# Kernel optimization log

Hardware: AMD Instinct MI355X
Metric: run time of the kernel (lower is better)

The kernel has to match this reference:

```python
import jax, jax.numpy as jnp
import numpy as np

B, S, D = 1, 4096, 512
QK_DIM, N_HEADS = 512, 8
HEAD_DIM = QK_DIM // N_HEADS


def setup_inputs() -> dict:
    key = jax.random.key(0)
    ks = jax.random.split(key, 9)
    s_in = 1.0 / np.sqrt(D)
    s_v = 1.0 / np.sqrt(QK_DIM)
    return {
        "x": jax.random.normal(ks[0], (B, S, D), dtype=jnp.float32),
        # torch nn.Linear convention: weight (out_features, in_features)
        "Wq": jax.random.uniform(ks[1], (QK_DIM, D), jnp.float32, -s_in, s_in),
        "bq": jax.random.uniform(ks[2], (QK_DIM,), jnp.float32, -s_in, s_in),
        "Wk": jax.random.uniform(ks[3], (QK_DIM, D), jnp.float32, -s_in, s_in),
        "bk": jax.random.uniform(ks[4], (QK_DIM,), jnp.float32, -s_in, s_in),
        "Wv": jax.random.uniform(ks[5], (QK_DIM, D), jnp.float32, -s_in, s_in),
        "bv": jax.random.uniform(ks[6], (QK_DIM,), jnp.float32, -s_in, s_in),
        "Wo": jax.random.uniform(ks[7], (D, QK_DIM), jnp.float32, -s_v, s_v),
        "bo": jax.random.uniform(ks[8], (D,), jnp.float32, -s_v, s_v),
    }


def reference(x, Wq, bq, Wk, bk, Wv, bv, Wo, bo):
    # Faithful to source: tokens flattened over batch*seq before head split.
    n = x.shape[0] * x.shape[1]  # B*S
    Q = (x @ Wq.T + bq).reshape(n, N_HEADS, HEAD_DIM).transpose(1, 0, 2)  # (H, N, hd)
    K = (x @ Wk.T + bk).reshape(n, N_HEADS, HEAD_DIM).transpose(1, 0, 2)
    V = (x @ Wv.T + bv).reshape(n, N_HEADS, HEAD_DIM).transpose(1, 0, 2)
    scores = jnp.einsum("hnd,hmd->hnm", Q, K) / np.sqrt(HEAD_DIM).astype(np.float32)
    attn = jax.nn.softmax(scores, axis=-1)                # (H, N, N) materialized
    ctx = jnp.einsum("hnm,hmd->hnd", attn, V)             # (H, N, hd)
    ctx = ctx.transpose(1, 0, 2).reshape(n, QK_DIM)       # (N, qk_dim)
    return ctx @ Wo.T + bo                                # (N, input_dim)
```

## Files before the change

### kernel.cpp

```cpp
#include <hip/hip_runtime.h>
#include <math.h>

#define N_TOK 4096
#define DMODEL 512
#define NH 8
#define HD 64

typedef __attribute__((ext_vector_type(4))) float f32x4;
typedef __attribute__((ext_vector_type(8))) _Float16 f16x8;
typedef __attribute__((ext_vector_type(4))) _Float16 f16x4;

#define MFMA16(A, B, C) __builtin_amdgcn_mfma_f32_16x16x32_f16(A, B, C, 0, 0, 0)

__global__ __launch_bounds__(256) void cast_x(const float* __restrict__ x,
                                              _Float16* __restrict__ X16) {
    int i = (blockIdx.x * 256 + threadIdx.x) * 8;
    f32x4 a = *(const f32x4*)&x[i];
    f32x4 b = *(const f32x4*)&x[i + 4];
    f16x8 o = {(_Float16)a[0], (_Float16)a[1], (_Float16)a[2], (_Float16)a[3],
               (_Float16)b[0], (_Float16)b[1], (_Float16)b[2], (_Float16)b[3]};
    *(f16x8*)&X16[i] = o;
}

__global__ __launch_bounds__(768) void qkv_gemm(const _Float16* __restrict__ X16,
                                                const float* __restrict__ Wq,
                                                const float* __restrict__ bq,
                                                const float* __restrict__ Wk,
                                                const float* __restrict__ bk,
                                                const float* __restrict__ Wv,
                                                const float* __restrict__ bv,
                                                _Float16* __restrict__ Q16,
                                                _Float16* __restrict__ K16,
                                                _Float16* __restrict__ VT16) {
    __shared__ __align__(16) _Float16 smem[46080];
    _Float16* AsB = smem;
    _Float16* WsB = smem + 18432;

    int t = threadIdx.x;
    int w = t >> 6, l = t & 63, quad = l >> 4, ln = l & 15;
    int z = w >> 2, ww = w & 3;
    int n0 = blockIdx.x * 128, o0 = blockIdx.y * 64;
    int h = o0 >> 6;

    const float* biasz = (z == 0) ? bq : (z == 1) ? bk : bv;

    f32x4 acc[2][4] = {};

    bool isA = (t < 256);
    int asr = t >> 3, asc = (t & 7) * 8;
    int tt = t - 256;
    int wr = tt >> 3, wc = (tt & 7) * 8;

    const _Float16* Abase = X16 + (size_t)n0 * DMODEL;
    const float* W0 = Wq + (size_t)o0 * DMODEL;
    const float* W1 = Wk + (size_t)o0 * DMODEL;
    const float* W2 = Wv + (size_t)o0 * DMODEL;

    f16x8 pa[4];
    f32x4 pw[3][2];
    if (isA) {
#pragma unroll
        for (int r = 0; r < 4; r++)
            pa[r] = *(const f16x8*)&Abase[(size_t)(asr + r * 32) * DMODEL + asc];
    } else {
        pw[0][0] = *(const f32x4*)&W0[(size_t)wr * DMODEL + wc];
        pw[0][1] = *(const f32x4*)&W0[(size_t)wr * DMODEL + wc + 4];
        pw[1][0] = *(const f32x4*)&W1[(size_t)wr * DMODEL + wc];
        pw[1][1] = *(const f32x4*)&W1[(size_t)wr * DMODEL + wc + 4];
        pw[2][0] = *(const f32x4*)&W2[(size_t)wr * DMODEL + wc];
        pw[2][1] = *(const f32x4*)&W2[(size_t)wr * DMODEL + wc + 4];
    }

    for (int it = 0; it < 8; it++) {
        int p = it & 1;
        if (isA) {
#pragma unroll
            for (int r = 0; r < 4; r++)
                *(f16x8*)&AsB[(size_t)(p * 128 + asr + r * 32) * 72 + asc] = pa[r];
        } else {
#pragma unroll
            for (int zt = 0; zt < 3; zt++) {
                f16x8 wv_ = {(_Float16)pw[zt][0][0], (_Float16)pw[zt][0][1],
                             (_Float16)pw[zt][0][2], (_Float16)pw[zt][0][3],
                             (_Float16)pw[zt][1][0], (_Float16)pw[zt][1][1],
                             (_Float16)pw[zt][1][2], (_Float16)pw[zt][1][3]};
                *(f16x8*)&WsB[(size_t)((p * 3 + zt) * 64 + wr) * 72 + wc] = wv_;
            }
        }
        __syncthreads();

        int k1 = (it + 1) * 64;
        if (k1 < DMODEL) {
            if (isA) {
#pragma unroll
                for (int r = 0; r < 4; r++)
                    pa[r] = *(const f16x8*)&Abase[(size_t)(asr + r * 32) * DMODEL + k1 + asc];
            } else {
                pw[0][0] = *(const f32x4*)&W0[(size_t)wr * DMODEL + k1 + wc];
                pw[0][1] = *(const f32x4*)&W0[(size_t)wr * DMODEL + k1 + wc + 4];
                pw[1][0] = *(const f32x4*)&W1[(size_t)wr * DMODEL + k1 + wc];
                pw[1][1] = *(const f32x4*)&W1[(size_t)wr * DMODEL + k1 + wc + 4];
                pw[2][0] = *(const f32x4*)&W2[(size_t)wr * DMODEL + k1 + wc];
                pw[2][1] = *(const f32x4*)&W2[(size_t)wr * DMODEL + k1 + wc + 4];
            }
        }

#pragma unroll
        for (int ks = 0; ks < 2; ks++) {
            f16x8 af0 = *(const f16x8*)&AsB[(size_t)(p * 128 + ww * 32 + ln) * 72 +
                                            ks * 32 + quad * 8];
            f16x8 af1 = *(const f16x8*)&AsB[(size_t)(p * 128 + ww * 32 + 16 + ln) * 72 +
                                            ks * 32 + quad * 8];
#pragma unroll
            for (int c = 0; c < 4; c++) {
                f16x8 bf = *(const f16x8*)&WsB[(size_t)((p * 3 + z) * 64 + c * 16 + ln) * 72 +
                                               ks * 32 + quad * 8];
                acc[0][c] = MFMA16(af0, bf, acc[0][c]);
                acc[1][c] = MFMA16(af1, bf, acc[1][c]);
            }
        }
    }

    __syncthreads();

    const float QS = 0.125f * 1.44269504088896340736f;
    _Float16* Qs = smem;
    _Float16* Ksep = smem + 9216;
    _Float16* Vt = smem + 18432;

    if (z < 2) {
        _Float16* st = (z == 0) ? Qs : Ksep;
        float sc_ = (z == 0) ? QS : 1.0f;
#pragma unroll
        for (int c = 0; c < 4; c++) {
            float bv_ = biasz[o0 + c * 16 + ln];
#pragma unroll
            for (int rt = 0; rt < 2; rt++)
#pragma unroll
                for (int i = 0; i < 4; i++) {
                    int lr = ww * 32 + rt * 16 + quad * 4 + i;
                    st[(size_t)lr * 72 + c * 16 + ln] =
                        (_Float16)((acc[rt][c][i] + bv_) * sc_);
                }
        }
    } else {
#pragma unroll
        for (int c = 0; c < 4; c++) {
            float bv_ = biasz[o0 + c * 16 + ln];
#pragma unroll
            for (int rt = 0; rt < 2; rt++)
#pragma unroll
                for (int i = 0; i < 4; i++) {
                    int np = (ww >> 1) * 64 + (quad * 4 + i) * 4 + (ww & 1) * 2 + rt;
                    Vt[(size_t)(c * 16 + ln) * 136 + np] = (_Float16)(acc[rt][c][i] + bv_);
                }
        }
    }
    __syncthreads();

    if (t < 256) {
#pragma unroll
        for (int k = 0; k < 4; k++) {
            int row = k * 32 + (t >> 3), col = (t & 7) * 8;
            *(f16x8*)&Q16[((size_t)h * N_TOK + n0 + row) * HD + col] =
                *(const f16x8*)&Qs[(size_t)row * 72 + col];
        }
    } else if (t < 512) {
        int u = t - 256;
#pragma unroll
        for (int k = 0; k < 4; k++) {
            int row = k * 32 + (u >> 3), col = (u & 7) * 8;
            *(f16x8*)&K16[((size_t)h * N_TOK + n0 + row) * HD + col] =
                *(const f16x8*)&Ksep[(size_t)row * 72 + col];
        }
    } else {
        int u = t - 512;
#pragma unroll
        for (int k = 0; k < 4; k++) {
            int d = k * 16 + (u >> 4), col = (u & 15) * 8;
            *(f16x8*)&VT16[((size_t)h * HD + d) * N_TOK + n0 + col] =
                *(const f16x8*)&Vt[(size_t)d * 136 + col];
        }
    }
}

#define SWZ(r, c) (((r) * 64) + ((c) ^ (((r) & 7) << 3)))

__global__ __launch_bounds__(1024) void flash_mfma(const _Float16* __restrict__ Q16,
                                                   const _Float16* __restrict__ K16,
                                                   const _Float16* __restrict__ VT16,
                                                   _Float16* __restrict__ OP,
                                                   float* __restrict__ LS) {
    __shared__ __align__(16) _Float16 Ks[2][64 * 64];
    __shared__ __align__(16) _Float16 Vs[2][64 * 64];
    __shared__ __align__(16) _Float16 Ps[16][32 * 64];

    int t = threadIdx.x;
    int w = t >> 6, l = t & 63, quad = l >> 4, ln = l & 15;
    int bid = blockIdx.x;
    int h = bid & 7;
    int qt = (bid >> 3) & 7;
    int s = bid >> 6;
    int q0 = qt * 512 + w * 32;
    int m_start = s * 1024;

    f16x8 qf[2][2];
#pragma unroll
    for (int rt = 0; rt < 2; rt++) {
        const _Float16* qp = &Q16[((size_t)h * N_TOK + q0 + rt * 16 + ln) * HD + quad * 8];
        qf[rt][0] = *(const f16x8*)qp;
        qf[rt][1] = *(const f16x8*)(qp + 32);
    }

    f32x4 oacc[2][4] = {};
    f32x4 lsum[2] = {};

    const _Float16* kbase = K16 + (size_t)h * N_TOK * HD;
    const _Float16* vbase = VT16 + (size_t)h * HD * N_TOK;
    int g = t >> 9, tt = t & 511;
    int srow = tt >> 3, scol = (tt & 7) * 8;

    f16x8 pkv;
    if (g == 0)
        pkv = *(const f16x8*)(kbase + (size_t)(m_start + srow) * HD + scol);
    else
        pkv = *(const f16x8*)(vbase + (size_t)srow * N_TOK + m_start + scol);

    for (int it = 0; it < 16; it++) {
        int m0 = m_start + it * 64;
        int p = it & 1;
        if (g == 0)
            *(f16x8*)&Ks[p][SWZ(srow, scol)] = pkv;
        else
            *(f16x8*)&Vs[p][SWZ(srow, scol)] = pkv;
        __syncthreads();

        if (it < 15) {
            int m1 = m0 + 64;
            if (g == 0)
                pkv = *(const f16x8*)(kbase + (size_t)(m1 + srow) * HD + scol);
            else
                pkv = *(const f16x8*)(vbase + (size_t)srow * N_TOK + m1 + scol);
        }

        f16x8 kb[4][2];
#pragma unroll
        for (int c = 0; c < 4; c++) {
            kb[c][0] = *(const f16x8*)&Ks[p][SWZ(c * 16 + ln, quad * 8)];
            kb[c][1] = *(const f16x8*)&Ks[p][SWZ(c * 16 + ln, 32 + quad * 8)];
        }
#pragma unroll
        for (int rt = 0; rt < 2; rt++) {
            f32x4 sacc[4] = {};
#pragma unroll
            for (int c = 0; c < 4; c++) {
                sacc[c] = MFMA16(qf[rt][0], kb[c][0], sacc[c]);
                sacc[c] = MFMA16(qf[rt][1], kb[c][1], sacc[c]);
            }
#pragma unroll
            for (int i = 0; i < 4; i++) {
                float p0 = __builtin_exp2f(sacc[0][i]);
                float p1 = __builtin_exp2f(sacc[1][i]);
                float p2 = __builtin_exp2f(sacc[2][i]);
                float p3 = __builtin_exp2f(sacc[3][i]);
                lsum[rt][i] += (p0 + p1) + (p2 + p3);
                f16x4 pvv = {(_Float16)p0, (_Float16)p1, (_Float16)p2, (_Float16)p3};
                *(f16x4*)&Ps[w][SWZ(rt * 16 + quad * 4 + i, ln * 4)] = pvv;
            }
        }
        f16x8 vb[4][2];
#pragma unroll
        for (int c = 0; c < 4; c++) {
            vb[c][0] = *(const f16x8*)&Vs[p][SWZ(c * 16 + ln, quad * 8)];
            vb[c][1] = *(const f16x8*)&Vs[p][SWZ(c * 16 + ln, 32 + quad * 8)];
        }
#pragma unroll
        for (int rt = 0; rt < 2; rt++) {
            f16x8 a0 = *(const f16x8*)&Ps[w][SWZ(rt * 16 + ln, quad * 8)];
            f16x8 a1 = *(const f16x8*)&Ps[w][SWZ(rt * 16 + ln, 32 + quad * 8)];
#pragma unroll
            for (int c = 0; c < 4; c++) {
                oacc[rt][c] = MFMA16(a0, vb[c][0], oacc[rt][c]);
                oacc[rt][c] = MFMA16(a1, vb[c][1], oacc[rt][c]);
            }
        }
    }

#pragma unroll
    for (int d = 1; d < 16; d <<= 1)
#pragma unroll
        for (int rt = 0; rt < 2; rt++)
#pragma unroll
            for (int i = 0; i < 4; i++) lsum[rt][i] += __shfl_xor(lsum[rt][i], d, 64);

    _Float16* obase = OP + (size_t)s * N_TOK * DMODEL;
#pragma unroll
    for (int rt = 0; rt < 2; rt++)
#pragma unroll
        for (int c = 0; c < 4; c++)
#pragma unroll
            for (int i = 0; i < 4; i++) {
                int r = q0 + rt * 16 + quad * 4 + i;
                obase[(size_t)r * DMODEL + h * HD + c * 16 + ln] = (_Float16)oacc[rt][c][i];
            }
    if (ln == 0) {
#pragma unroll
        for (int rt = 0; rt < 2; rt++)
#pragma unroll
            for (int i = 0; i < 4; i++) {
                int r = q0 + rt * 16 + quad * 4 + i;
                LS[((size_t)s * NH + h) * N_TOK + r] = lsum[rt][i];
            }
    }
}

__global__ __launch_bounds__(512) void out_gemm(const _Float16* __restrict__ OP,
                                                const float* __restrict__ LS,
                                                const float* __restrict__ Wo,
                                                const float* __restrict__ bo,
                                                float* __restrict__ out) {
    __shared__ __align__(16) _Float16 smem[27648];
    _Float16* AsB = smem;
    _Float16* WsB = smem + 18432;

    int t = threadIdx.x;
    int w = t >> 6, l = t & 63, quad = l >> 4, ln = l & 15;
    int n0 = blockIdx.x * 128, o0 = blockIdx.y * 64;
    int sr = t >> 2, sc = (t & 3) * 16;
    int wr = t >> 3, wc = (t & 7) * 8;
    const size_t PSTR = (size_t)N_TOK * DMODEL;

    f32x4 acc[4] = {};

    const float* Wbase = Wo + (size_t)o0 * DMODEL;

    f16x8 pa[4][2];
    float lt;
    f32x4 pw0, pw1;
    {
        size_t base = (size_t)(n0 + sr) * DMODEL + sc;
#pragma unroll
        for (int s_ = 0; s_ < 4; s_++) {
            pa[s_][0] = *(const f16x8*)&OP[s_ * PSTR + base];
            pa[s_][1] = *(const f16x8*)&OP[s_ * PSTR + base + 8];
        }
        const float* ls = LS + n0 + sr;
        lt = (ls[0] + ls[NH * N_TOK]) + (ls[2 * NH * N_TOK] + ls[3 * NH * N_TOK]);
        pw0 = *(const f32x4*)&Wbase[(size_t)wr * DMODEL + wc];
        pw1 = *(const f32x4*)&Wbase[(size_t)wr * DMODEL + wc + 4];
    }

    for (int it = 0; it < 8; it++) {
        int p = it & 1;
        {
            float inv = 1.0f / lt;
            f16x8 s0, s1;
#pragma unroll
            for (int j = 0; j < 8; j++) {
                s0[j] = (_Float16)(
                    ((((float)pa[0][0][j] + (float)pa[1][0][j]) +
                      ((float)pa[2][0][j] + (float)pa[3][0][j]))) * inv);
                s1[j] = (_Float16)(
                    ((((float)pa[0][1][j] + (float)pa[1][1][j]) +
                      ((float)pa[2][1][j] + (float)pa[3][1][j]))) * inv);
            }
            *(f16x8*)&AsB[(size_t)(p * 128 + sr) * 72 + sc] = s0;
            *(f16x8*)&AsB[(size_t)(p * 128 + sr) * 72 + sc + 8] = s1;
            f16x8 wv_ = {(_Float16)pw0[0], (_Float16)pw0[1], (_Float16)pw0[2],
                         (_Float16)pw0[3], (_Float16)pw1[0], (_Float16)pw1[1],
                         (_Float16)pw1[2], (_Float16)pw1[3]};
            *(f16x8*)&WsB[(size_t)(p * 64 + wr) * 72 + wc] = wv_;
        }
        __syncthreads();

        int k1 = (it + 1) * 64;
        if (k1 < DMODEL) {
            int h1 = k1 >> 6;
            size_t base = (size_t)(n0 + sr) * DMODEL + k1 + sc;
#pragma unroll
            for (int s_ = 0; s_ < 4; s_++) {
                pa[s_][0] = *(const f16x8*)&OP[s_ * PSTR + base];
                pa[s_][1] = *(const f16x8*)&OP[s_ * PSTR + base + 8];
            }
            const float* ls = LS + (size_t)h1 * N_TOK + n0 + sr;
            lt = (ls[0] + ls[NH * N_TOK]) + (ls[2 * NH * N_TOK] + ls[3 * NH * N_TOK]);
            pw0 = *(const f32x4*)&Wbase[(size_t)wr * DMODEL + k1 + wc];
            pw1 = *(const f32x4*)&Wbase[(size_t)wr * DMODEL + k1 + wc + 4];
        }

#pragma unroll
        for (int ks = 0; ks < 2; ks++) {
            f16x8 af = *(const f16x8*)&AsB[(size_t)(p * 128 + w * 16 + ln) * 72 +
                                           ks * 32 + quad * 8];
#pragma unroll
            for (int c = 0; c < 4; c++) {
                f16x8 bf = *(const f16x8*)&WsB[(size_t)(p * 64 + c * 16 + ln) * 72 +
                                               ks * 32 + quad * 8];
                acc[c] = MFMA16(af, bf, acc[c]);
            }
        }
    }

#pragma unroll
    for (int c = 0; c < 4; c++) {
        float bv_ = bo[o0 + c * 16 + ln];
#pragma unroll
        for (int i = 0; i < 4; i++) {
            int r = n0 + w * 16 + quad * 4 + i;
            out[(size_t)r * DMODEL + o0 + c * 16 + ln] = acc[c][i] + bv_;
        }
    }
}

extern "C" void kernel_launch(void* const* d_in, const int* in_sizes, int n_in,
                              void* d_out, int out_size, void* d_ws, size_t ws_size,
                              hipStream_t stream) {
    const float* x  = (const float*)d_in[0];
    const float* Wq = (const float*)d_in[1];
    const float* bq = (const float*)d_in[2];
    const float* Wk = (const float*)d_in[3];
    const float* bk = (const float*)d_in[4];
    const float* Wv = (const float*)d_in[5];
    const float* bv = (const float*)d_in[6];
    const float* Wo = (const float*)d_in[7];
    const float* bo = (const float*)d_in[8];
    float* out = (float*)d_out;

    char* ws = (char*)d_ws;
    _Float16* X16  = (_Float16*)(ws);
    _Float16* Q16  = (_Float16*)(ws + (4u << 20));
    _Float16* K16  = (_Float16*)(ws + (8u << 20));
    _Float16* VT16 = (_Float16*)(ws + (12u << 20));
    _Float16* OP   = (_Float16*)(ws + (16u << 20));
    float*    LSp  = (float*)   (ws + (32u << 20));

    cast_x<<<1024, 256, 0, stream>>>(x, X16);

    qkv_gemm<<<dim3(32, 8), 768, 0, stream>>>(X16, Wq, bq, Wk, bk, Wv, bv,
                                              Q16, K16, VT16);

    flash_mfma<<<dim3(256), 1024, 0, stream>>>(Q16, K16, VT16, OP, LSp);

    out_gemm<<<dim3(32, 8), 512, 0, stream>>>(OP, LSp, Wo, bo, out);
}
```

Before: 158.2 us.

## Keep P in registers by computing transposed S and O tiles

Swaps the MFMA operand order so the score tile is computed transposed (K as A, Q as B). Each lane then holds exponentiated P values in exactly the layout needed as the B operand of the P·V MFMA, so the per-wave shared-memory P staging buffer and its stores and loads are removed. The V transpose layout written by the QKV kernel is permuted to match the new key ordering inside each 64-key tile. Row sums need only two cross-lane shuffles, and output stores become 4-wide vectors along the head dimension. This trades LDS traffic and about 64KB of LDS for a coupled layout change across two kernels that must stay consistent.

New measurement: 155.9 us. No clear change (-1.5%).

```diff
diff --git a/kernel.cpp b/kernel.cpp
--- a/kernel.cpp
+++ b/kernel.cpp
@@ -151,7 +151,7 @@
             for (int rt = 0; rt < 2; rt++)
 #pragma unroll
                 for (int i = 0; i < 4; i++) {
-                    int np = (ww >> 1) * 64 + (quad * 4 + i) * 4 + (ww & 1) * 2 + rt;
+                    int np = (ww >> 1) * 64 + (ww & 1) * 32 + quad * 8 + rt * 4 + i;
                     Vt[(size_t)(c * 16 + ln) * 136 + np] = (_Float16)(acc[rt][c][i] + bv_);
                 }
         }
@@ -193,7 +193,6 @@
                                                    float* __restrict__ LS) {
     __shared__ __align__(16) _Float16 Ks[2][64 * 64];
     __shared__ __align__(16) _Float16 Vs[2][64 * 64];
-    __shared__ __align__(16) _Float16 Ps[16][32 * 64];
 
     int t = threadIdx.x;
     int w = t >> 6, l = t & 63, quad = l >> 4, ln = l & 15;
@@ -213,7 +212,7 @@
     }
 
     f32x4 oacc[2][4] = {};
-    f32x4 lsum[2] = {};
+    float lsum[2] = {0.0f, 0.0f};
 
     const _Float16* kbase = K16 + (size_t)h * N_TOK * HD;
     const _Float16* vbase = VT16 + (size_t)h * HD * N_TOK;
@@ -249,68 +248,66 @@
             kb[c][0] = *(const f16x8*)&Ks[p][SWZ(c * 16 + ln, quad * 8)];
             kb[c][1] = *(const f16x8*)&Ks[p][SWZ(c * 16 + ln, 32 + quad * 8)];
         }
+
+        f16x8 bf[2][2];
 #pragma unroll
         for (int rt = 0; rt < 2; rt++) {
             f32x4 sacc[4] = {};
 #pragma unroll
-            for (int c = 0; c < 4; c++) {
-                sacc[c] = MFMA16(qf[rt][0], kb[c][0], sacc[c]);
-                sacc[c] = MFMA16(qf[rt][1], kb[c][1], sacc[c]);
-            }
-#pragma unroll
-            for (int i = 0; i < 4; i++) {
-                float p0 = __builtin_exp2f(sacc[0][i]);
-                float p1 = __builtin_exp2f(sacc[1][i]);
-                float p2 = __builtin_exp2f(sacc[2][i]);
-                float p3 = __builtin_exp2f(sacc[3][i]);
-                lsum[rt][i] += (p0 + p1) + (p2 + p3);
-                f16x4 pvv = {(_Float16)p0, (_Float16)p1, (_Float16)p2, (_Float16)p3};
-                *(f16x4*)&Ps[w][SWZ(rt * 16 + quad * 4 + i, ln * 4)] = pvv;
-            }
-        }
-        f16x8 vb[4][2];
+            for (int kk = 0; kk < 4; kk++) {
+                sacc[kk] = MFMA16(kb[kk][0], qf[rt][0], sacc[kk]);
+                sacc[kk] = MFMA16(kb[kk][1], qf[rt][1], sacc[kk]);
+            }
+            float ls0 = 0.0f;
+#pragma unroll
+            for (int kk = 0; kk < 4; kk++) {
+                float e0 = __builtin_exp2f(sacc[kk][0]);
+                float e1 = __builtin_exp2f(sacc[kk][1]);
+                float e2 = __builtin_exp2f(sacc[kk][2]);
+                float e3 = __builtin_exp2f(sacc[kk][3]);
+                ls0 += (e0 + e1) + (e2 + e3);
+                bf[rt][kk >> 1][(kk & 1) * 4 + 0] = (_Float16)e0;
+                bf[rt][kk >> 1][(kk & 1) * 4 + 1] = (_Float16)e1;
+                bf[rt][kk >> 1][(kk & 1) * 4 + 2] = (_Float16)e2;
+                bf[rt][kk >> 1][(kk & 1) * 4 + 3] = (_Float16)e3;
+            }
+            lsum[rt] += ls0;
+        }
+
 #pragma unroll
         for (int c = 0; c < 4; c++) {
-            vb[c][0] = *(const f16x8*)&Vs[p][SWZ(c * 16 + ln, quad * 8)];
-            vb[c][1] = *(const f16x8*)&Vs[p][SWZ(c * 16 + ln, 32 + quad * 8)];
-        }
+            f16x8 va0 = *(const f16x8*)&Vs[p][SWZ(c * 16 + ln, quad * 8)];
+            f16x8 va1 = *(const f16x8*)&Vs[p][SWZ(c * 16 + ln, 32 + quad * 8)];
+            oacc[0][c] = MFMA16(va0, bf[0][0], oacc[0][c]);
+            oacc[0][c] = MFMA16(va1, bf[0][1], oacc[0][c]);
+            oacc[1][c] = MFMA16(va0, bf[1][0], oacc[1][c]);
+            oacc[1][c] = MFMA16(va1, bf[1][1], oacc[1][c]);
+        }
+    }
+
+#pragma unroll
+    for (int rt = 0; rt < 2; rt++) {
+        lsum[rt] += __shfl_xor(lsum[rt], 16, 64);
+        lsum[rt] += __shfl_xor(lsum[rt], 32, 64);
+    }
+
+    _Float16* obase = OP + (size_t)s * N_TOK * DMODEL;
+#pragma unroll
+    for (int rt = 0; rt < 2; rt++) {
+        int r = q0 + rt * 16 + ln;
+#pragma unroll
+        for (int c = 0; c < 4; c++) {
+            f16x4 ov = {(_Float16)oacc[rt][c][0], (_Float16)oacc[rt][c][1],
+                        (_Float16)oacc[rt][c][2], (_Float16)oacc[rt][c][3]};
+            *(f16x4*)&obase[(size_t)r * DMODEL + h * HD + c * 16 + quad * 4] = ov;
+        }
+    }
+    if (l < 16) {
 #pragma unroll
         for (int rt = 0; rt < 2; rt++) {
-            f16x8 a0 = *(const f16x8*)&Ps[w][SWZ(rt * 16 + ln, quad * 8)];
-            f16x8 a1 = *(const f16x8*)&Ps[w][SWZ(rt * 16 + ln, 32 + quad * 8)];
-#pragma unroll
-            for (int c = 0; c < 4; c++) {
-                oacc[rt][c] = MFMA16(a0, vb[c][0], oacc[rt][c]);
-                oacc[rt][c] = MFMA16(a1, vb[c][1], oacc[rt][c]);
-            }
-        }
-    }
-
-#pragma unroll
-    for (int d = 1; d < 16; d <<= 1)
-#pragma unroll
-        for (int rt = 0; rt < 2; rt++)
-#pragma unroll
-            for (int i = 0; i < 4; i++) lsum[rt][i] += __shfl_xor(lsum[rt][i], d, 64);
-
-    _Float16* obase = OP + (size_t)s * N_TOK * DMODEL;
-#pragma unroll
-    for (int rt = 0; rt < 2; rt++)
-#pragma unroll
-        for (int c = 0; c < 4; c++)
-#pragma unroll
-            for (int i = 0; i < 4; i++) {
-                int r = q0 + rt * 16 + quad * 4 + i;
-                obase[(size_t)r * DMODEL + h * HD + c * 16 + ln] = (_Float16)oacc[rt][c][i];
-            }
-    if (ln == 0) {
-#pragma unroll
-        for (int rt = 0; rt < 2; rt++)
-#pragma unroll
-            for (int i = 0; i < 4; i++) {
-                int r = q0 + rt * 16 + quad * 4 + i;
-                LS[((size_t)s * NH + h) * N_TOK + r] = lsum[rt][i];
-            }
+            int r = q0 + rt * 16 + ln;
+            LS[((size_t)s * NH + h) * N_TOK + r] = lsum[rt];
+        }
     }
 }
 
```
